# Kernel tuning notes

Hardware: AMD Instinct MI355X
Metric: run time of the kernel (lower is better)

## Reference

```python
import jax, jax.numpy as jnp
import numpy as np
from jax import lax

B, S, C_IN, D, H, P, W, DFF, K = 32, 4096, 32, 256, 8, 24, 64, 512, 5
DH = D // H
EPS = 1e-5


def _make_starts():
    stride = max(1, W // 2)
    idx = list(range(0, max(S - W + 1, 1), stride))
    if len(idx) == 0 or idx[-1] != S - W:
        if S - W >= 0:
            idx.append(S - W)
    return np.asarray(idx)

STARTS = _make_starts()                      # [M]
WIDX = STARTS[:, None] + np.arange(W)        # [M, W] patch gather indices


def setup_inputs() -> dict:
    key = jax.random.key(0)
    ks = jax.random.split(key, 24)
    r = lambda i, shape, s=0.02: (jax.random.normal(ks[i], shape, jnp.float32) * s)
    return {
        "x": jax.random.normal(ks[0], (B, S, C_IN), jnp.float32),
        "last_close_unused": jnp.zeros((B,), jnp.float32),
        "dw_w": r(1, (C_IN, 1, K), 0.2),      # depthwise conv kernel
        "pw_w": r(2, (D, C_IN), 0.1),         # pointwise conv (1x1)
        "bn_g": jnp.ones((D,), jnp.float32),
        "bn_b": jnp.zeros((D,), jnp.float32),
        "lg_Wq": r(3, (D, D)), "lg_Wk": r(4, (D, D)),
        "lg_Wv": r(5, (D, D)), "lg_Wo": r(6, (D, D)),
        "dec_Qd": r(7, (P, D), 1.0 / np.sqrt(D)),
        "dec_Wq": r(8, (D, D)), "dec_Wk": r(9, (D, D)),
        "dec_Wv": r(10, (D, D)), "dec_Wo": r(11, (D, D)),
        "ff1_w": r(12, (DFF, D)), "ff1_b": jnp.zeros((DFF,), jnp.float32),
        "ff2_w": r(13, (D, DFF)), "ff2_b": jnp.zeros((D,), jnp.float32),
        "out_w": r(14, (1, D)), "out_b": jnp.zeros((1,), jnp.float32),
        "gate_logits": jnp.tile(jnp.array([0.2, 0.4, 0.4], jnp.float32), (P, 1)),
    }


def _ln(x):
    m = x.mean(-1, keepdims=True)
    v = ((x - m) ** 2).mean(-1, keepdims=True)
    return (x - m) / jnp.sqrt(v + EPS)


def _split(t):  # [B, L, D] -> [B, H, L, DH]
    return t.reshape(t.shape[0], -1, H, DH).transpose(0, 2, 1, 3)


def _mha(Q, KV, Wq, Wk, Wv, scale):
    q = _split(Q @ Wq.T)
    k = _split(KV @ Wk.T)
    v = _split(KV @ Wv.T)
    attn = jax.nn.softmax(jnp.einsum('bhqd,bhkd->bhqk', q, k) * scale, axis=-1)
    o = jnp.einsum('bhqk,bhkd->bhqd', attn, v)
    o = o.transpose(0, 2, 1, 3).reshape(Q.shape[0], -1, D)
    return o, attn


def reference(x, last_close_unused, dw_w, pw_w, bn_g, bn_b,
              lg_Wq, lg_Wk, lg_Wv, lg_Wo,
              dec_Qd, dec_Wq, dec_Wk, dec_Wv, dec_Wo,
              ff1_w, ff1_b, ff2_w, ff2_b, out_w, out_b, gate_logits):
    # --- DepthwisePointwise front-end ---
    xt = jnp.transpose(x, (0, 2, 1))                         # [B, C, S]
    z = lax.conv_general_dilated(xt, dw_w, (1,), [(K // 2, K // 2)],
                                 dimension_numbers=('NCH', 'OIH', 'NCH'),
                                 feature_group_count=C_IN)
    z = jnp.einsum('dc,bcs->bds', pw_w, z)                   # pointwise 1x1
    z = jax.nn.gelu(z, approximate=False)
    m = z.mean((0, 2), keepdims=True)                        # BatchNorm1d (batch stats)
    v = ((z - m) ** 2).mean((0, 2), keepdims=True)
    z = (z - m) / jnp.sqrt(v + EPS) * bn_g[None, :, None] + bn_b[None, :, None]
    z = jnp.transpose(z, (0, 2, 1))                          # [B, S, D]

    # --- LocalGlobalAttention: patch-mean queries over full sequence K/V ---
    Q = z[:, WIDX].mean(axis=2)                              # [B, M, D]
    scale = 1.0 / np.sqrt(DH)
    o, attn_g = _mha(Q, z, lg_Wq, lg_Wk, lg_Wv, scale)
    Hh = _ln(o @ lg_Wo.T + Q)                                # [B, M, D]

    # --- CrossDecoder: learned queries ---
    Qd = jnp.broadcast_to(dec_Qd[None], (B, P, D))
    o2, attn_d = _mha(Qd, Hh, dec_Wq, dec_Wk, dec_Wv, scale)
    z2 = _ln(o2 @ dec_Wo.T + Qd)
    u = jax.nn.gelu(z2 @ ff1_w.T + ff1_b, approximate=False)
    u = _ln(u @ ff2_w.T + ff2_b + z2)
    y_global = (u @ out_w.T + out_b)[..., 0]                 # [B, P]

    # --- Gated combine: residual=0, local=global ---
    g = jax.nn.softmax(gate_logits, axis=-1)                 # [P, 3]
    y = g[:, 1][None, :] * y_global + g[:, 2][None, :] * y_global
    return (y, attn_g, attn_d)
```

## Files before the change

kernel.cpp:

```cpp
#include <hip/hip_runtime.h>
#include <hip/hip_bf16.h>
#include <cmath>

typedef unsigned short u16;
typedef __attribute__((ext_vector_type(4))) float f32x4;
typedef __attribute__((ext_vector_type(8))) short s16x8;

__device__ __forceinline__ float b2f(u16 u) { return __uint_as_float(((unsigned)u) << 16); }
__device__ __forceinline__ u16 f2b(float f) {
    unsigned u = __float_as_uint(f);
    unsigned r = (u + 0x7fffu + ((u >> 16) & 1u)) >> 16;
    return (u16)r;
}
__device__ __forceinline__ float gelu_f(float x) {
    float t = x * (0.7978845608f + 0.0356774081f * x * x);
    float e = exp2f(2.885390082f * t);
    return 0.5f * x * (1.0f + (e - 1.0f) / (e + 1.0f));
}

#define FOLD 0.25503590f

__global__ __launch_bounds__(256) void prep0_k(const float* __restrict__ pw_w,
        const float* __restrict__ lg_Wq, const float* __restrict__ lg_Wo,
        const float* __restrict__ dec_Wk, const float* __restrict__ dec_Wv,
// ... 58 lines not shown
    s16x8 bf[4];
    #pragma unroll
    for (int ni = 0; ni < 4; ++ni)
        bf[ni] = *(const s16x8*)(pwb + (n0 + ni * 16 + l16) * 32 + hi * 8);

    float cl[4] = {0,0,0,0}, ch[4] = {0,0,0,0};
    float ql[4] = {0,0,0,0}, qh[4] = {0,0,0,0};

    #pragma unroll
    for (int mi = 0; mi < 4; ++mi) {
        s16x8 af = *(const s16x8*)&As[mi * 16 + l16][hi * 8];
        #pragma unroll
        for (int ni = 0; ni < 4; ++ni) {
            f32x4 acc = __builtin_amdgcn_mfma_f32_16x16x32_bf16(af, bf[ni], zero, 0, 0, 0);
            int col = n0 + ni * 16 + l16;
            int rowb = r0 + mi * 16 + hi * 4;
            #pragma unroll
            for (int r = 0; r < 4; ++r) {
                float e = gelu_f(acc[r]);
                zp[(size_t)(rowb + r) * 256 + col] = f2b(e);
                if (mi < 2) { cl[ni] += e; ql[ni] += e * e; }
                else        { ch[ni] += e; qh[ni] += e * e; }
            }
        }
    }
    #pragma unroll
    for (int ni = 0; ni < 4; ++ni) {
        #pragma unroll
        for (int m = 16; m <= 32; m <<= 1) {
            cl[ni] += __shfl_xor(cl[ni], m);
            ch[ni] += __shfl_xor(ch[ni], m);
            ql[ni] += __shfl_xor(ql[ni], m);
            qh[ni] += __shfl_xor(qh[ni], m);
        }
        if (lane < 16) {
            int col = n0 + ni * 16 + lane;
            size_t bc = (size_t)(r0 >> 5);
            csum [bc * 256 + col]       = cl[ni];
            csum [(bc + 1) * 256 + col] = ch[ni];
            csum2[bc * 256 + col]       = ql[ni];
            csum2[(bc + 1) * 256 + col] = qh[ni];
        }
    }
}

__global__ __launch_bounds__(256) void stats2_k(const float* __restrict__ csum,
        const float* __restrict__ csum2, float* __restrict__ statp)
{
    int j = blockIdx.x, t = threadIdx.x;
    float s1 = 0, s2 = 0;
    for (int i = 0; i < 64; ++i) {
        s1 += csum [(size_t)(j * 64 + i) * 256 + t];
        s2 += csum2[(size_t)(j * 64 + i) * 256 + t];
    }
    statp[j * 512 + t] = s1;
    statp[j * 512 + 256 + t] = s2;
}

__global__ __launch_bounds__(256) void prep1_k(const float* __restrict__ statp,
        const float* __restrict__ bn_g, const float* __restrict__ bn_b,
        const float* __restrict__ gate_logits,
        float* __restrict__ a_ws, float* __restrict__ c_ws, float* __restrict__ coef)
{
    int t = threadIdx.x;
    float s1 = 0, s2 = 0;
    for (int j = 0; j < 64; ++j) {
        s1 += statp[j * 512 + t];
        s2 += statp[j * 512 + 256 + t];
    }
    const float invN = 1.0f / 131072.0f;
    float mean = s1 * invN;
    float var = s2 * invN - mean * mean;
    float av = bn_g[t] * rsqrtf(var + 1e-5f);
    a_ws[t] = av;
    c_ws[t] = bn_b[t] - mean * av;
    if (t < 24) {
        float g0 = gate_logits[t * 3], g1 = gate_logits[t * 3 + 1], g2 = gate_logits[t * 3 + 2];
        float mx = fmaxf(g0, fmaxf(g1, g2));
        float e0 = __expf(g0 - mx), e1 = __expf(g1 - mx), e2 = __expf(g2 - mx);
        coef[t] = (e1 + e2) / (e0 + e1 + e2);
    }
}

__global__ __launch_bounds__(256) void prep2b_k(const float* __restrict__ lg_Wk,
        const float* __restrict__ lg_Wv, const float* __restrict__ a_ws,
        const float* __restrict__ c_ws,
        u16* __restrict__ Wk_b, u16* __restrict__ Wv_b,
        float* __restrict__ betak, float* __restrict__ betav)
{
    __shared__ float red[4];
    int bid = blockIdx.x;
    int which = bid >> 8, row = bid & 255, t = threadIdx.x;
    const float* Wsrc = which ? lg_Wv : lg_Wk;
    float wv = Wsrc[row * 256 + t];
    (which ? Wv_b : Wk_b)[row * 256 + t] = f2b(wv * a_ws[t]);
    float v = wv * c_ws[t];
    for (int m = 32; m; m >>= 1) v += __shfl_xor(v, m);
    if ((t & 63) == 0) red[t >> 6] = v;
    __syncthreads();
    if (t == 0) (which ? betav : betak)[row] = red[0] + red[1] + red[2] + red[3];
}

__global__ __launch_bounds__(256) void q2_k(const float* __restrict__ dec_Qd,
        const float* __restrict__ dec_Wq, float* __restrict__ q2)
{
    __shared__ float wq[16][260];
    __shared__ float qd[24][260];
    int j = blockIdx.x, t = threadIdx.x;
    for (int idx = t; idx < 4096; idx += 256) {
        int tl = idx >> 8, d = idx & 255;
        wq[tl][d] = dec_Wq[(j * 16 + tl) * 256 + d];
    }
    for (int idx = t; idx < 6144; idx += 256) {
        int p = idx >> 8, d = idx & 255;
        qd[p][d] = dec_Qd[idx];
    }
    __syncthreads();
    for (int o = t; o < 384; o += 256) {
        int p = o >> 4, tl = o & 15;
        float s = 0;
        #pragma unroll 8
        for (int d = 0; d < 256; ++d) s += qd[p][d] * wq[tl][d];
        q2[p * 256 + j * 16 + tl] = s;
    }
}

__global__ __launch_bounds__(256) void qgemm_k(const float* __restrict__ csum,
        const float* __restrict__ a_ws, const float* __restrict__ c_ws,
        const u16* __restrict__ W, u16* __restrict__ qb)
{
    __shared__ u16 As[64 * 256];
    __shared__ float aa[256], ccx[256];
    const int t = threadIdx.x;
    const int r0 = blockIdx.x * 64;
    const int lane = t & 63, w = t >> 6;
    const int l16 = lane & 15, hi = lane >> 4;

    aa[t] = a_ws[t] * 0.015625f;
    ccx[t] = c_ws[t];
    __syncthreads();

    #pragma unroll
    for (int i = 0; i < 8; ++i) {
        int c = t + i * 256;
        int row = c >> 5, c16 = c & 31;
        int g = r0 + row, mm = g & 127;
        u16 tmp[8];
        if (mm == 127) {
            #pragma unroll
            for (int j = 0; j < 8; ++j) tmp[j] = 0;
        } else {
            const float* c0p = csum + (size_t)g * 256 + c16 * 8;
            const float* c1p = c0p + 256;
            #pragma unroll
            for (int j = 0; j < 8; ++j) {
                int d = c16 * 8 + j;
                tmp[j] = f2b((c0p[j] + c1p[j]) * aa[d] + ccx[d]);
            }
        }
        int boff = (c16 * 16) ^ ((row & 7) << 4);
        *(s16x8*)((char*)As + row * 512 + boff) = *(s16x8*)tmp;
    }
    __syncthreads();

    const int n0 = w * 64;
    f32x4 zero = {0, 0, 0, 0};
    f32x4 acc[4][4];
    #pragma unroll
    for (int mi = 0; mi < 4; ++mi)
        #pragma unroll
        for (int ni = 0; ni < 4; ++ni) acc[mi][ni] = zero;

    #pragma unroll
    for (int kk = 0; kk < 8; ++kk) {
        s16x8 af[4], bf[4];
        #pragma unroll
        for (int mi = 0; mi < 4; ++mi) {
            int row = mi * 16 + l16;
            int boff = (kk * 64 + hi * 16) ^ ((row & 7) << 4);
            af[mi] = *(const s16x8*)((const char*)As + row * 512 + boff);
        }
        #pragma unroll
        for (int ni = 0; ni < 4; ++ni)
            bf[ni] = *(const s16x8*)(W + (n0 + ni * 16 + l16) * 256 + kk * 32 + hi * 8);
        #pragma unroll
        for (int mi = 0; mi < 4; ++mi)
            #pragma unroll
            for (int ni = 0; ni < 4; ++ni)
                acc[mi][ni] = __builtin_amdgcn_mfma_f32_16x16x32_bf16(af[mi], bf[ni], acc[mi][ni], 0, 0, 0);
    }

    #pragma unroll
    for (int mi = 0; mi < 4; ++mi)
        #pragma unroll
        for (int ni = 0; ni < 4; ++ni) {
            int col = n0 + ni * 16 + l16;
            int rowb = r0 + mi * 16 + hi * 4;
            #pragma unroll
            for (int r = 0; r < 4; ++r)
                qb[(size_t)(rowb + r) * 256 + col] = f2b(acc[mi][ni][r] * FOLD);
        }
}

__global__ __launch_bounds__(256) void kv_k(const u16* __restrict__ zp,
        const u16* __restrict__ Wk, const u16* __restrict__ Wv,
        const float* __restrict__ betak, const float* __restrict__ betav,
        u16* __restrict__ kb, u16* __restrict__ vT)
{
    __shared__ __align__(16) char smem[36864];
    u16* As = (u16*)smem;
    const int t = threadIdx.x;
    const int r0 = blockIdx.x * 64;
    const int lane = t & 63, w = t >> 6;
    const int l16 = lane & 15, hi = lane >> 4;

    const u16* Ag = zp + (size_t)r0 * 256;
    #pragma unroll
    for (int i = 0; i < 8; ++i) {
        int c = t + i * 256;
        int row = c >> 5, c16 = c & 31;
        s16x8 v = *(const s16x8*)(Ag + row * 256 + c16 * 8);
        int boff = (c16 * 16) ^ ((row & 7) << 4);
        *(s16x8*)(smem + row * 512 + boff) = v;
    }
    __syncthreads();

    const int n0 = w * 64;
    f32x4 zero = {0, 0, 0, 0};
    f32x4 acc[4][4];
    #pragma unroll
    for (int mi = 0; mi < 4; ++mi)
        #pragma unroll
        for (int ni = 0; ni < 4; ++ni) acc[mi][ni] = zero;

    #pragma unroll
    for (int kk = 0; kk < 8; ++kk) {
        s16x8 af[4], bfk[4];
        #pragma unroll
        for (int mi = 0; mi < 4; ++mi) {
            int row = mi * 16 + l16;
            int boff = (kk * 64 + hi * 16) ^ ((row & 7) << 4);
            af[mi] = *(const s16x8*)(smem + row * 512 + boff);
        }
        #pragma unroll
        for (int ni = 0; ni < 4; ++ni)
            bfk[ni] = *(const s16x8*)(Wk + (n0 + ni * 16 + l16) * 256 + kk * 32 + hi * 8);
        #pragma unroll
        for (int mi = 0; mi < 4; ++mi)
            #pragma unroll
            for (int ni = 0; ni < 4; ++ni)
                acc[mi][ni] = __builtin_amdgcn_mfma_f32_16x16x32_bf16(af[mi], bfk[ni], acc[mi][ni], 0, 0, 0);
    }
    #pragma unroll
    for (int mi = 0; mi < 4; ++mi)
        #pragma unroll
        for (int ni = 0; ni < 4; ++ni) {
            int col = n0 + ni * 16 + l16;
            float bv = betak[col];
            int rowb = r0 + mi * 16 + hi * 4;
            #pragma unroll
            for (int r = 0; r < 4; ++r)
                kb[(size_t)(rowb + r) * 256 + col] = f2b(acc[mi][ni][r] + bv);
        }

    #pragma unroll
    for (int mi = 0; mi < 4; ++mi)
        #pragma unroll
        for (int ni = 0; ni < 4; ++ni) acc[mi][ni] = zero;
    #pragma unroll
    for (int kk = 0; kk < 8; ++kk) {
        s16x8 af[4], bfv[4];
        #pragma unroll
        for (int mi = 0; mi < 4; ++mi) {
            int row = mi * 16 + l16;
            int boff = (kk * 64 + hi * 16) ^ ((row & 7) << 4);
            af[mi] = *(const s16x8*)(smem + row * 512 + boff);
        }
        #pragma unroll
        for (int ni = 0; ni < 4; ++ni)
            bfv[ni] = *(const s16x8*)(Wv + (n0 + ni * 16 + l16) * 256 + kk * 32 + hi * 8);
        #pragma unroll
        for (int mi = 0; mi < 4; ++mi)
            #pragma unroll
            for (int ni = 0; ni < 4; ++ni)
                acc[mi][ni] = __builtin_amdgcn_mfma_f32_16x16x32_bf16(af[mi], bfv[ni], acc[mi][ni], 0, 0, 0);
    }
    __syncthreads();
    #pragma unroll
    for (int mi = 0; mi < 4; ++mi)
        #pragma unroll
        for (int ni = 0; ni < 4; ++ni) {
            int col = n0 + ni * 16 + l16;
            float bv = betav[col];
// ... 142 lines not shown
            for (int ni = 0; ni < 4; ++ni)
                acc[mi][ni] = __builtin_amdgcn_mfma_f32_16x16x32_bf16(af[mi], bf[ni], acc[mi][ni], 0, 0, 0);
    }
    #pragma unroll
    for (int mi = 0; mi < 4; ++mi)
        #pragma unroll
        for (int ni = 0; ni < 4; ++ni) {
            int col = n0 + ni * 16 + l16;
            int rowb = r0 + mi * 16 + hi * 4;
            #pragma unroll
            for (int r = 0; r < 4; ++r)
                C[(size_t)(rowb + r) * 256 + col] = f2b(acc[mi][ni][r]);
        }
}

__global__ __launch_bounds__(512) void attn_p1(const u16* __restrict__ qb,
        const u16* __restrict__ kb, const u16* __restrict__ vT,
        float* __restrict__ den, float* __restrict__ o_part)
{
    const int bid = blockIdx.x;
    const int b = bid >> 6, h = (bid >> 3) & 7, chunk = bid & 7;
    const int t = threadIdx.x, w = t >> 6, lane = t & 63;
    const int l16 = lane & 15, hi = lane >> 4;

    __shared__ u16 p_lds[8][16][48];

    s16x8 qf = *(const s16x8*)(qb + ((size_t)(b * 128 + w * 16 + l16)) * 256 + h * 32 + hi * 8);
    const u16* kbase = kb + (size_t)b * 4096 * 256 + h * 32 + hi * 8;
    const u16* vbase = vT + (size_t)(b * 8 + h) * 131072 + hi * 8;

    float dacc[4] = {0, 0, 0, 0};
    f32x4 zero = {0, 0, 0, 0};
    f32x4 oacc[2]; oacc[0] = zero; oacc[1] = zero;

    const int sbeg = chunk * 512, send = sbeg + 512;
    s16x8 kf0 = *(const s16x8*)(kbase + (size_t)(sbeg + l16) * 256);
    s16x8 kf1 = *(const s16x8*)(kbase + (size_t)(sbeg + 16 + l16) * 256);
    s16x8 vf0 = *(const s16x8*)(vbase + (sbeg >> 6) * 2048 + l16 * 64 + (sbeg & 63));
    s16x8 vf1 = *(const s16x8*)(vbase + (sbeg >> 6) * 2048 + (16 + l16) * 64 + (sbeg & 63));

    for (int s0 = sbeg; s0 < send; s0 += 32) {
        s16x8 k0 = kf0, k1 = kf1, v0 = vf0, v1 = vf1;
        int sn = s0 + 32;
        if (sn < send) {
            kf0 = *(const s16x8*)(kbase + (size_t)(sn + l16) * 256);
            kf1 = *(const s16x8*)(kbase + (size_t)(sn + 16 + l16) * 256);
            vf0 = *(const s16x8*)(vbase + (sn >> 6) * 2048 + l16 * 64 + (sn & 63));
            vf1 = *(const s16x8*)(vbase + (sn >> 6) * 2048 + (16 + l16) * 64 + (sn & 63));
        }
        f32x4 lg0 = __builtin_amdgcn_mfma_f32_16x16x32_bf16(qf, k0, zero, 0, 0, 0);
        f32x4 lg1 = __builtin_amdgcn_mfma_f32_16x16x32_bf16(qf, k1, zero, 0, 0, 0);
        #pragma unroll
        for (int r = 0; r < 4; ++r) {
            float e0 = exp2f(lg0[r]);
            float e1 = exp2f(lg1[r]);
            dacc[r] += e0 + e1;
            p_lds[w][hi * 4 + r][l16] = f2b(e0);
            p_lds[w][hi * 4 + r][16 + l16] = f2b(e1);
        }
        s16x8 pf = *(const s16x8*)(&p_lds[w][l16][hi * 8]);
        oacc[0] = __builtin_amdgcn_mfma_f32_16x16x32_bf16(pf, v0, oacc[0], 0, 0, 0);
        oacc[1] = __builtin_amdgcn_mfma_f32_16x16x32_bf16(pf, v1, oacc[1], 0, 0, 0);
    }

    #pragma unroll
    for (int m = 1; m <= 8; m <<= 1) {
        #pragma unroll
        for (int r = 0; r < 4; ++r) dacc[r] += __shfl_xor(dacc[r], m);
    }
    if (l16 == 0) {
        #pragma unroll
        for (int r = 0; r < 4; ++r)
            den[(size_t)chunk * 32768 + (b * 8 + h) * 128 + w * 16 + hi * 4 + r] = dacc[r];
    }
    #pragma unroll
    for (int vi = 0; vi < 2; ++vi)
        #pragma unroll
        for (int r = 0; r < 4; ++r) {
            int mg = w * 16 + hi * 4 + r;
            o_part[(size_t)chunk * 1048576 + (size_t)(b * 128 + mg) * 256 + h * 32 + vi * 16 + l16] = oacc[vi][r];
        }
}

__global__ __launch_bounds__(256) void dinv_k(const float* __restrict__ den, float* __restrict__ den_inv)
{
    int i = blockIdx.x * 256 + threadIdx.x;
    float s = 0;
    #pragma unroll
    for (int c = 0; c < 8; ++c) s += den[(size_t)c * 32768 + i];
    den_inv[i] = 1.0f / s;
}

__global__ __launch_bounds__(256) void norm_k(const float* __restrict__ o_part,
        const float* __restrict__ den_inv, u16* __restrict__ ob)
{
    int idx4 = blockIdx.x * 256 + threadIdx.x;
    int row = idx4 >> 6;
    int col4 = (idx4 & 63) * 4;
    int b = row >> 7, m = row & 127, h = col4 >> 5;
    float4 s = {0, 0, 0, 0};
    #pragma unroll
    for (int c = 0; c < 8; ++c) {
        float4 v = *(const float4*)(o_part + (size_t)c * 1048576 + (size_t)row * 256 + col4);
        s.x += v.x; s.y += v.y; s.z += v.z; s.w += v.w;
    }
    float rinv = den_inv[b * 1024 + h * 128 + m];
    ushort4 o;
    o.x = f2b(s.x * rinv); o.y = f2b(s.y * rinv);
    o.z = f2b(s.z * rinv); o.w = f2b(s.w * rinv);
    *(ushort4*)(ob + (size_t)row * 256 + col4) = o;
}

__global__ __launch_bounds__(512) void attn_p2(const u16* __restrict__ qb,
        const u16* __restrict__ kb, const float* __restrict__ den_inv,
        float* __restrict__ attn_out)
{
    const int bid = blockIdx.x;
    const int b = bid >> 6, h = (bid >> 3) & 7, chunk = bid & 7;
    const int t = threadIdx.x, w = t >> 6, lane = t & 63;
    const int l16 = lane & 15, hi = lane >> 4;

    __shared__ float buf[8][16][68];

    s16x8 qf = *(const s16x8*)(qb + ((size_t)(b * 128 + w * 16 + l16)) * 256 + h * 32 + hi * 8);
    const u16* kbase = kb + (size_t)b * 4096 * 256 + h * 32 + hi * 8;

    float rinv[4];
    #pragma unroll
    for (int r = 0; r < 4; ++r)
        rinv[r] = den_inv[b * 1024 + h * 128 + w * 16 + hi * 4 + r];

    f32x4 zero = {0, 0, 0, 0};
    float* ab = attn_out + (size_t)(b * 8 + h) * 127 * 4096;
    const int srow = lane >> 4;
    const int scol = (lane & 15) * 4;

    const int sbeg = chunk * 512, send = sbeg + 512;
    for (int s0 = sbeg; s0 < send; s0 += 64) {
        #pragma unroll
        for (int kk = 0; kk < 4; ++kk) {
            int sg = s0 + kk * 16 + l16;
            s16x8 kf = *(const s16x8*)(kbase + (size_t)sg * 256);
            f32x4 lg = __builtin_amdgcn_mfma_f32_16x16x32_bf16(qf, kf, zero, 0, 0, 0);
            #pragma unroll
            for (int r = 0; r < 4; ++r)
                buf[w][hi * 4 + r][kk * 16 + l16] = exp2f(lg[r]) * rinv[r];
        }
        #pragma unroll
        for (int rb = 0; rb < 4; ++rb) {
            int row = rb * 4 + srow;
            int mg = w * 16 + row;
            float4 v = *(const float4*)&buf[w][row][scol];
            if (mg < 127)
                *(float4*)(ab + (size_t)mg * 4096 + s0 + scol) = v;
        }
    }
}

__global__ __launch_bounds__(256) void ln_hh(const float* __restrict__ og,
        const float* __restrict__ csum, const float* __restrict__ a_ws,
        const float* __restrict__ c_ws, u16* __restrict__ Hb)
{
    __shared__ float red[8];
    int row = blockIdx.x, t = threadIdx.x;
    int mm = row & 127;
    float qv = 0.0f;
    if (mm != 127)
        qv = (csum[(size_t)row * 256 + t] + csum[(size_t)(row + 1) * 256 + t]) *
             (0.015625f * a_ws[t]) + c_ws[t];
    float v = og[(size_t)row * 256 + t] + qv;
    float s = v;
    for (int m = 32; m; m >>= 1) s += __shfl_xor(s, m);
    if ((t & 63) == 0) red[t >> 6] = s;
    __syncthreads();
    float mean = (red[0] + red[1] + red[2] + red[3]) * (1.0f / 256.0f);
    __syncthreads();
    float d = v - mean;
    float q = d * d;
    for (int m = 32; m; m >>= 1) q += __shfl_xor(q, m);
    if ((t & 63) == 0) red[t >> 6] = q;
    __syncthreads();
    float var = (red[0] + red[1] + red[2] + red[3]) * (1.0f / 256.0f);
    Hb[(size_t)row * 256 + t] = f2b(d * rsqrtf(var + 1e-5f));
}

__global__ __launch_bounds__(256) void dec_attn_k(const float* __restrict__ q2,
        const u16* __restrict__ k2b, const u16* __restrict__ v2b,
        float* __restrict__ attn_d, u16* __restrict__ o2b)
{
    __shared__ float qs2[24 * 32];
    __shared__ float ks[128][33];
    __shared__ float vs[128][33];
    __shared__ float lg2[24 * 128];
    __shared__ float sinv[24];
    int bid = blockIdx.x, b = bid >> 3, h = bid & 7;
    int t = threadIdx.x;
    const float scale = 0.17677669529663687f;
    for (int idx = t; idx < 4096; idx += 256) {
        int row = idx >> 5, c = idx & 31;
        ks[row][c] = b2f(k2b[((size_t)(b * 128 + row)) * 256 + h * 32 + c]);
        vs[row][c] = b2f(v2b[((size_t)(b * 128 + row)) * 256 + h * 32 + c]);
    }
    for (int idx = t; idx < 768; idx += 256) {
        int p = idx >> 5, i = idx & 31;
        qs2[idx] = q2[p * 256 + h * 32 + i];
    }
    __syncthreads();
    for (int idx = t; idx < 3048; idx += 256) {
        int p = idx / 127, m = idx - p * 127;
        float s = 0;
        #pragma unroll 8
        for (int i = 0; i < 32; ++i) s += qs2[p * 32 + i] * ks[m][i];
        lg2[p * 128 + m] = __expf(s * scale);
    }
    __syncthreads();
    if (t < 24) {
        float s = 0;
        for (int m = 0; m < 127; ++m) s += lg2[t * 128 + m];
        sinv[t] = 1.0f / s;
    }
    __syncthreads();
    float* ad = attn_d + (size_t)bid * 24 * 127;
    for (int idx = t; idx < 3048; idx += 256) {
        int p = idx / 127, m = idx - p * 127;
        float av = lg2[p * 128 + m] * sinv[p];
        lg2[p * 128 + m] = av;
        ad[idx] = av;
    }
    __syncthreads();
    for (int idx = t; idx < 768; idx += 256) {
        int p = idx >> 5, dh = idx & 31;
        float s = 0;
        for (int m = 0; m < 127; ++m)
            s += lg2[p * 128 + m] * vs[m][dh];
        o2b[((size_t)(b * 24 + p)) * 256 + h * 32 + dh] = f2b(s);
    }
}

__global__ __launch_bounds__(256) void ln3_k(const float* __restrict__ og2,
        const float* __restrict__ dec_Qd, float* __restrict__ z2f, u16* __restrict__ z2b)
{
    __shared__ float red[8];
    int row = blockIdx.x, p = row % 24, t = threadIdx.x;
    float v = og2[(size_t)row * 256 + t] + dec_Qd[p * 256 + t];
    float s = v;
    for (int m = 32; m; m >>= 1) s += __shfl_xor(s, m);
    if ((t & 63) == 0) red[t >> 6] = s;
    __syncthreads();
    float mean = (red[0] + red[1] + red[2] + red[3]) * (1.0f / 256.0f);
    __syncthreads();
    float d = v - mean, q = d * d;
    for (int m = 32; m; m >>= 1) q += __shfl_xor(q, m);
    if ((t & 63) == 0) red[t >> 6] = q;
    __syncthreads();
    float var = (red[0] + red[1] + red[2] + red[3]) * (1.0f / 256.0f);
    float u = d * rsqrtf(var + 1e-5f);
    z2f[(size_t)row * 256 + t] = u;
    z2b[(size_t)row * 256 + t] = f2b(u);
}

__global__ __launch_bounds__(256) void ln5_k(const float* __restrict__ uraw,
        const float* __restrict__ z2f, const float* __restrict__ out_w,
        const float* __restrict__ out_b, const float* __restrict__ coef,
        float* __restrict__ y)
{
    __shared__ float red[8];
    int row = blockIdx.x, p = row % 24, t = threadIdx.x;
    float v = uraw[(size_t)row * 256 + t] + z2f[(size_t)row * 256 + t];
    float s = v;
    for (int m = 32; m; m >>= 1) s += __shfl_xor(s, m);
    if ((t & 63) == 0) red[t >> 6] = s;
    __syncthreads();
    float mean = (red[0] + red[1] + red[2] + red[3]) * (1.0f / 256.0f);
    __syncthreads();
    float d = v - mean, q = d * d;
    for (int m = 32; m; m >>= 1) q += __shfl_xor(q, m);
    if ((t & 63) == 0) red[t >> 6] = q;
    __syncthreads();
    float var = (red[0] + red[1] + red[2] + red[3]) * (1.0f / 256.0f);
    float u = d * rsqrtf(var + 1e-5f);
    __syncthreads();
    float yp = u * out_w[t];
    for (int m = 32; m; m >>= 1) yp += __shfl_xor(yp, m);
    if ((t & 63) == 0) red[t >> 6] = yp;
    __syncthreads();
    if (t == 0) {
        float tot = red[0] + red[1] + red[2] + red[3] + out_b[0];
        y[row] = coef[p] * tot;
    }
}

extern "C" void kernel_launch(void* const* d_in, const int* in_sizes, int n_in,
                              void* d_out, int out_size, void* d_ws, size_t ws_size,
                              hipStream_t stream)
{
    const float* x        = (const float*)d_in[0];
    const float* dw_w     = (const float*)d_in[2];
    const float* pw_w     = (const float*)d_in[3];
    const float* bn_g     = (const float*)d_in[4];
    const float* bn_b     = (const float*)d_in[5];
    const float* lg_Wq    = (const float*)d_in[6];
    const float* lg_Wk    = (const float*)d_in[7];
    const float* lg_Wv    = (const float*)d_in[8];
    const float* lg_Wo    = (const float*)d_in[9];
    const float* dec_Qd   = (const float*)d_in[10];
    const float* dec_Wq   = (const float*)d_in[11];
    const float* dec_Wk   = (const float*)d_in[12];
    const float* dec_Wv   = (const float*)d_in[13];
    const float* dec_Wo   = (const float*)d_in[14];
    const float* ff1_w    = (const float*)d_in[15];
    const float* ff1_b    = (const float*)d_in[16];
    const float* ff2_w    = (const float*)d_in[17];
    const float* ff2_b    = (const float*)d_in[18];
    const float* out_w    = (const float*)d_in[19];
    const float* out_b    = (const float*)d_in[20];
    const float* gate_lg  = (const float*)d_in[21];

    char* ws = (char*)d_ws;
    size_t off = 0;
    auto alloc = [&](size_t bytes) -> void* {
        void* p = ws + off;
        off = (off + bytes + 255) & ~(size_t)255;
        return p;
    };
    u16*   zp    = (u16*)  alloc(67108864);
    u16*   kb    = (u16*)  alloc(67108864);
    u16*   vT    = (u16*)  alloc(67108864);
    float* csum  = (float*)alloc(4194304);
    float* csum2 = (float*)alloc(4194304);
    u16*   qb    = (u16*)  alloc(2097152);
    u16*   ob    = (u16*)  alloc(2097152);
    float* og    = (float*)alloc(4194304);
    u16*   Hb    = (u16*)  alloc(2097152);
    u16*   k2b   = (u16*)  alloc(2097152);
    u16*   v2b   = (u16*)  alloc(2097152);
    float* o_part= (float*)alloc(33554432);
    u16*   o2b   = (u16*)  alloc(393216);
    float* og2   = (float*)alloc(786432);
    float* z2f   = (float*)alloc(786432);
    u16*   z2b   = (u16*)  alloc(393216);
    u16*   u1b   = (u16*)  alloc(786432);
    float* uraw  = (float*)alloc(786432);
    float* q2    = (float*)alloc(24576);
    float* den   = (float*)alloc(1048576);
    float* den_i = (float*)alloc(131072);
    float* statp = (float*)alloc(131072);
    float* a_ws  = (float*)alloc(1024);
    float* c_ws  = (float*)alloc(1024);
    float* betak = (float*)alloc(1024);
    float* betav = (float*)alloc(1024);
    float* coef  = (float*)alloc(256);
    u16*   pwb   = (u16*)  alloc(16384);
    u16*   Wk_b  = (u16*)  alloc(131072);
    u16*   Wv_b  = (u16*)  alloc(131072);
    u16*   Wq_b  = (u16*)  alloc(131072);
    u16*   Wo_b  = (u16*)  alloc(131072);
    u16*   Wk2_b = (u16*)  alloc(131072);
    u16*   Wv2_b = (u16*)  alloc(131072);
    u16*   Wo2b  = (u16*)  alloc(131072);
    u16*   ff1b  = (u16*)  alloc(262144);
    u16*   ff2b  = (u16*)  alloc(262144);

    float* y_out  = (float*)d_out;
    float* attn_g = y_out + 768;
    float* attn_d = attn_g + (size_t)32 * 8 * 127 * 4096;

    prep0_k<<<2336, 256, 0, stream>>>(pw_w, lg_Wq, lg_Wo, dec_Wk, dec_Wv, dec_Wo, ff1_w, ff2_w,
                                      pwb, Wq_b, Wo_b, Wk2_b, Wv2_b, Wo2b, ff1b, ff2b);
    dwpw_k<<<2048, 256, 0, stream>>>(x, dw_w, pwb, zp, csum, csum2);
    stats2_k<<<64, 256, 0, stream>>>(csum, csum2, statp);
    prep1_k<<<1, 256, 0, stream>>>(statp, bn_g, bn_b, gate_lg, a_ws, c_ws, coef);
    prep2b_k<<<512, 256, 0, stream>>>(lg_Wk, lg_Wv, a_ws, c_ws, Wk_b, Wv_b, betak, betav);
    q2_k<<<16, 256, 0, stream>>>(dec_Qd, dec_Wq, q2);
    qgemm_k<<<64, 256, 0, stream>>>(csum, a_ws, c_ws, Wq_b, qb);
    kv_k<<<2048, 256, 0, stream>>>(zp, Wk_b, Wv_b, betak, betav, kb, vT);
    attn_p1<<<2048, 512, 0, stream>>>(qb, kb, vT, den, o_part);
    dinv_k<<<128, 256, 0, stream>>>(den, den_i);
    norm_k<<<1024, 256, 0, stream>>>(o_part, den_i, ob);
    attn_p2<<<2048, 512, 0, stream>>>(qb, kb, den_i, attn_g);
    gemm_g<1><<<64, 256, 0, stream>>>(ob, Wo_b, nullptr, og, 256, 1);
    ln_hh<<<4096, 256, 0, stream>>>(og, csum, a_ws, c_ws, Hb);
    gemm_dual<<<128, 256, 0, stream>>>(Hb, Wk2_b, Wv2_b, k2b, v2b);
    dec_attn_k<<<256, 256, 0, stream>>>(q2, k2b, v2b, attn_d, o2b);
    gemm_g<1><<<12, 256, 0, stream>>>(o2b, Wo2b, nullptr, og2, 256, 1);
    ln3_k<<<768, 256, 0, stream>>>(og2, dec_Qd, z2f, z2b);
    gemm_g<2><<<24, 256, 0, stream>>>(z2b, ff1b, ff1_b, u1b, 256, 2);
    gemm_g<1><<<12, 256, 0, stream>>>(u1b, ff2b, ff2_b, uraw, 512, 1);
    ln5_k<<<768, 256, 0, stream>>>(uraw, z2f, out_w, out_b, coef, y_out);
}
```

Before: 563.5 us.

## Fuse small prep kernels and merge layernorms into GEMM epilogues

Merges the prep2b, q2 and qgemm kernels into one launch that branches on block index, and folds the denominator reciprocal into norm_k and attn_p2 so dinv_k is gone. The three post-GEMM layernorm kernels (ln_hh, ln3, ln5) become epilogues of their GEMMs through a shared-memory staging tile, which drops the fp32 intermediate buffers. This removes several kernel launches and global round-trips on the small tail stages. In exchange the layernorm work now runs on far fewer blocks (64 or 12), and the denominator sum over chunks is recomputed in every thread.

After: 601.2 us. 6.7% more time.

```diff
diff --git a/kernel.cpp b/kernel.cpp
--- a/kernel.cpp
+++ b/kernel.cpp
@@ -164,124 +164,116 @@
     }
 }
 
-__global__ __launch_bounds__(256) void prep2b_k(const float* __restrict__ lg_Wk,
+__global__ __launch_bounds__(256) void prepx_k(const float* __restrict__ lg_Wk,
         const float* __restrict__ lg_Wv, const float* __restrict__ a_ws,
-        const float* __restrict__ c_ws,
+        const float* __restrict__ c_ws, const float* __restrict__ dec_Qd,
+        const float* __restrict__ dec_Wq, const float* __restrict__ csum,
+        const u16* __restrict__ Wq_b,
         u16* __restrict__ Wk_b, u16* __restrict__ Wv_b,
-        float* __restrict__ betak, float* __restrict__ betav)
-{
-    __shared__ float red[4];
-    int bid = blockIdx.x;
-    int which = bid >> 8, row = bid & 255, t = threadIdx.x;
-    const float* Wsrc = which ? lg_Wv : lg_Wk;
-    float wv = Wsrc[row * 256 + t];
-    (which ? Wv_b : Wk_b)[row * 256 + t] = f2b(wv * a_ws[t]);
-    float v = wv * c_ws[t];
-    for (int m = 32; m; m >>= 1) v += __shfl_xor(v, m);
-    if ((t & 63) == 0) red[t >> 6] = v;
-    __syncthreads();
-    if (t == 0) (which ? betav : betak)[row] = red[0] + red[1] + red[2] + red[3];
-}
-
-__global__ __launch_bounds__(256) void q2_k(const float* __restrict__ dec_Qd,
-        const float* __restrict__ dec_Wq, float* __restrict__ q2)
-{
-    __shared__ float wq[16][260];
-    __shared__ float qd[24][260];
-    int j = blockIdx.x, t = threadIdx.x;
-    for (int idx = t; idx < 4096; idx += 256) {
-        int tl = idx >> 8, d = idx & 255;
-        wq[tl][d] = dec_Wq[(j * 16 + tl) * 256 + d];
-    }
-    for (int idx = t; idx < 6144; idx += 256) {
-        int p = idx >> 8, d = idx & 255;
-        qd[p][d] = dec_Qd[idx];
-    }
-    __syncthreads();
-    for (int o = t; o < 384; o += 256) {
-        int p = o >> 4, tl = o & 15;
-        float s = 0;
-        #pragma unroll 8
-        for (int d = 0; d < 256; ++d) s += qd[p][d] * wq[tl][d];
-        q2[p * 256 + j * 16 + tl] = s;
-    }
-}
-
-__global__ __launch_bounds__(256) void qgemm_k(const float* __restrict__ csum,
-        const float* __restrict__ a_ws, const float* __restrict__ c_ws,
-        const u16* __restrict__ W, u16* __restrict__ qb)
-{
-    __shared__ u16 As[64 * 256];
-    __shared__ float aa[256], ccx[256];
-    const int t = threadIdx.x;
-    const int r0 = blockIdx.x * 64;
-    const int lane = t & 63, w = t >> 6;
-    const int l16 = lane & 15, hi = lane >> 4;
-
-    aa[t] = a_ws[t] * 0.015625f;
-    ccx[t] = c_ws[t];
-    __syncthreads();
-
-    #pragma unroll
-    for (int i = 0; i < 8; ++i) {
-        int c = t + i * 256;
-        int row = c >> 5, c16 = c & 31;
-        int g = r0 + row, mm = g & 127;
-        u16 tmp[8];
-        if (mm == 127) {
-            #pragma unroll
-            for (int j = 0; j < 8; ++j) tmp[j] = 0;
-        } else {
-            const float* c0p = csum + (size_t)g * 256 + c16 * 8;
-            const float* c1p = c0p + 256;
-            #pragma unroll
-            for (int j = 0; j < 8; ++j) {
-                int d = c16 * 8 + j;
-                tmp[j] = f2b((c0p[j] + c1p[j]) * aa[d] + ccx[d]);
+        float* __restrict__ betak, float* __restrict__ betav,
+        float* __restrict__ q2, u16* __restrict__ qb)
+{
+    __shared__ __align__(16) char sm[41728];
+    const int bid = blockIdx.x, t = threadIdx.x;
+    if (bid < 512) {
+        float* red = (float*)sm;
+        int which = bid >> 8, row = bid & 255;
+        const float* Wsrc = which ? lg_Wv : lg_Wk;
+        float wv = Wsrc[row * 256 + t];
+        (which ? Wv_b : Wk_b)[row * 256 + t] = f2b(wv * a_ws[t]);
+        float v = wv * c_ws[t];
+        for (int m = 32; m; m >>= 1) v += __shfl_xor(v, m);
+        if ((t & 63) == 0) red[t >> 6] = v;
+        __syncthreads();
+        if (t == 0) (which ? betav : betak)[row] = red[0] + red[1] + red[2] + red[3];
+    } else if (bid < 528) {
+        float (*wq)[260] = (float(*)[260])sm;
+        float (*qd)[260] = (float(*)[260])(sm + 16640);
+        int j = bid - 512;
+        for (int idx = t; idx < 4096; idx += 256) {
+            int tl = idx >> 8, d = idx & 255;
+            wq[tl][d] = dec_Wq[(j * 16 + tl) * 256 + d];
+        }
+        for (int idx = t; idx < 6144; idx += 256) {
+            int p = idx >> 8, d = idx & 255;
+            qd[p][d] = dec_Qd[idx];
+        }
+        __syncthreads();
+        for (int o = t; o < 384; o += 256) {
+            int p = o >> 4, tl = o & 15;
+            float s = 0;
+            #pragma unroll 8
+            for (int d = 0; d < 256; ++d) s += qd[p][d] * wq[tl][d];
+            q2[p * 256 + j * 16 + tl] = s;
+        }
+    } else {
+        u16* As = (u16*)sm;
+        float* aa = (float*)(sm + 32768);
+        float* ccx = (float*)(sm + 33792);
+        const int r0 = (bid - 528) * 64;
+        const int lane = t & 63, w = t >> 6;
+        const int l16 = lane & 15, hi = lane >> 4;
+        aa[t] = a_ws[t] * 0.015625f;
+        ccx[t] = c_ws[t];
+        __syncthreads();
+        #pragma unroll
+        for (int i = 0; i < 8; ++i) {
+            int c = t + i * 256;
+            int row = c >> 5, c16 = c & 31;
+            int g = r0 + row, mm = g & 127;
+            u16 tmp[8];
+            if (mm == 127) {
+                #pragma unroll
+                for (int j = 0; j < 8; ++j) tmp[j] = 0;
+            } else {
+                const float* c0p = csum + (size_t)g * 256 + c16 * 8;
+                const float* c1p = c0p + 256;
+                #pragma unroll
+                for (int j = 0; j < 8; ++j) {
+                    int d = c16 * 8 + j;
+                    tmp[j] = f2b((c0p[j] + c1p[j]) * aa[d] + ccx[d]);
+                }
             }
-        }
-        int boff = (c16 * 16) ^ ((row & 7) << 4);
-        *(s16x8*)((char*)As + row * 512 + boff) = *(s16x8*)tmp;
-    }
-    __syncthreads();
-
-    const int n0 = w * 64;
-    f32x4 zero = {0, 0, 0, 0};
-    f32x4 acc[4][4];
-    #pragma unroll
-    for (int mi = 0; mi < 4; ++mi)
-        #pragma unroll
-        for (int ni = 0; ni < 4; ++ni) acc[mi][ni] = zero;
-
-    #pragma unroll
-    for (int kk = 0; kk < 8; ++kk) {
-        s16x8 af[4], bf[4];
-        #pragma unroll
-        for (int mi = 0; mi < 4; ++mi) {
-            int row = mi * 16 + l16;
-            int boff = (kk * 64 + hi * 16) ^ ((row & 7) << 4);
-            af[mi] = *(const s16x8*)((const char*)As + row * 512 + boff);
-        }
-        #pragma unroll
-        for (int ni = 0; ni < 4; ++ni)
-            bf[ni] = *(const s16x8*)(W + (n0 + ni * 16 + l16) * 256 + kk * 32 + hi * 8);
+            int boff = (c16 * 16) ^ ((row & 7) << 4);
+            *(s16x8*)((char*)As + row * 512 + boff) = *(s16x8*)tmp;
+        }
+        __syncthreads();
+        const int n0 = w * 64;
+        f32x4 zero = {0, 0, 0, 0};
+        f32x4 acc[4][4];
         #pragma unroll
         for (int mi = 0; mi < 4; ++mi)
             #pragma unroll
+            for (int ni = 0; ni < 4; ++ni) acc[mi][ni] = zero;
+        #pragma unroll
+        for (int kk = 0; kk < 8; ++kk) {
+            s16x8 af[4], bf[4];
+            #pragma unroll
+            for (int mi = 0; mi < 4; ++mi) {
+                int row = mi * 16 + l16;
+                int boff = (kk * 64 + hi * 16) ^ ((row & 7) << 4);
+                af[mi] = *(const s16x8*)((const char*)As + row * 512 + boff);
+            }
+            #pragma unroll
             for (int ni = 0; ni < 4; ++ni)
-                acc[mi][ni] = __builtin_amdgcn_mfma_f32_16x16x32_bf16(af[mi], bf[ni], acc[mi][ni], 0, 0, 0);
-    }
-
-    #pragma unroll
-    for (int mi = 0; mi < 4; ++mi)
-        #pragma unroll
-        for (int ni = 0; ni < 4; ++ni) {
-            int col = n0 + ni * 16 + l16;
-            int rowb = r0 + mi * 16 + hi * 4;
-            #pragma unroll
-            for (int r = 0; r < 4; ++r)
-                qb[(size_t)(rowb + r) * 256 + col] = f2b(acc[mi][ni][r] * FOLD);
-        }
+                bf[ni] = *(const s16x8*)(Wq_b + (n0 + ni * 16 + l16) * 256 + kk * 32 + hi * 8);
+            #pragma unroll
+            for (int mi = 0; mi < 4; ++mi)
+                #pragma unroll
+                for (int ni = 0; ni < 4; ++ni)
+                    acc[mi][ni] = __builtin_amdgcn_mfma_f32_16x16x32_bf16(af[mi], bf[ni], acc[mi][ni], 0, 0, 0);
+        }
+        #pragma unroll
+        for (int mi = 0; mi < 4; ++mi)
+            #pragma unroll
+            for (int ni = 0; ni < 4; ++ni) {
+                int col = n0 + ni * 16 + l16;
+                int rowb = r0 + mi * 16 + hi * 4;
+                #pragma unroll
+                for (int r = 0; r < 4; ++r)
+                    qb[(size_t)(rowb + r) * 256 + col] = f2b(acc[mi][ni][r] * FOLD);
+            }
+    }
 }
 
 __global__ __launch_bounds__(256) void kv_k(const u16* __restrict__ zp,
@@ -290,7 +282,6 @@
         u16* __restrict__ kb, u16* __restrict__ vT)
 {
     __shared__ __align__(16) char smem[36864];
-    u16* As = (u16*)smem;
     const int t = threadIdx.x;
     const int r0 = blockIdx.x * 64;
     const int lane = t & 63, w = t >> 6;
@@ -599,37 +590,30 @@
         }
 }
 
-__global__ __launch_bounds__(256) void dinv_k(const float* __restrict__ den, float* __restrict__ den_inv)
-{
-    int i = blockIdx.x * 256 + threadIdx.x;
-    float s = 0;
-    #pragma unroll
-    for (int c = 0; c < 8; ++c) s += den[(size_t)c * 32768 + i];
-    den_inv[i] = 1.0f / s;
-}
-
 __global__ __launch_bounds__(256) void norm_k(const float* __restrict__ o_part,
-        const float* __restrict__ den_inv, u16* __restrict__ ob)
+        const float* __restrict__ den, u16* __restrict__ ob)
 {
     int idx4 = blockIdx.x * 256 + threadIdx.x;
     int row = idx4 >> 6;
     int col4 = (idx4 & 63) * 4;
     int b = row >> 7, m = row & 127, h = col4 >> 5;
-    float4 s = {0, 0, 0, 0};
-    #pragma unroll
-    for (int c = 0; c < 8; ++c) {
-        float4 v = *(const float4*)(o_part + (size_t)c * 1048576 + (size_t)row * 256 + col4);
-        s.x += v.x; s.y += v.y; s.z += v.z; s.w += v.w;
-    }
-    float rinv = den_inv[b * 1024 + h * 128 + m];
+    f32x4 s = {0, 0, 0, 0};
+    #pragma unroll
+    for (int c = 0; c < 8; ++c)
+        s += *(const f32x4*)(o_part + (size_t)c * 1048576 + (size_t)row * 256 + col4);
+    float ds = 0;
+    int di = (b * 8 + h) * 128 + m;
+    #pragma unroll
+    for (int c = 0; c < 8; ++c) ds += den[(size_t)c * 32768 + di];
+    float rinv = 1.0f / ds;
     ushort4 o;
-    o.x = f2b(s.x * rinv); o.y = f2b(s.y * rinv);
-    o.z = f2b(s.z * rinv); o.w = f2b(s.w * rinv);
+    o.x = f2b(s[0] * rinv); o.y = f2b(s[1] * rinv);
+    o.z = f2b(s[2] * rinv); o.w = f2b(s[3] * rinv);
     *(ushort4*)(ob + (size_t)row * 256 + col4) = o;
 }
 
 __global__ __launch_bounds__(512) void attn_p2(const u16* __restrict__ qb,
-        const u16* __restrict__ kb, const float* __restrict__ den_inv,
+        const u16* __restrict__ kb, const float* __restrict__ den,
         float* __restrict__ attn_out)
 {
     const int bid = blockIdx.x;
@@ -644,8 +628,13 @@
 
     float rinv[4];
     #pragma unroll
-    for (int r = 0; r < 4; ++r)
-        rinv[r] = den_inv[b * 1024 + h * 128 + w * 16 + hi * 4 + r];
+    for (int r = 0; r < 4; ++r) {
+        int di = (b * 8 + h) * 128 + w * 16 + hi * 4 + r;
+        float ds = 0;
+        #pragma unroll
+        for (int c = 0; c < 8; ++c) ds += den[(size_t)c * 32768 + di];
+        rinv[r] = 1.0f / ds;
+    }
 
     f32x4 zero = {0, 0, 0, 0};
     float* ab = attn_out + (size_t)(b * 8 + h) * 127 * 4096;
@@ -667,38 +656,102 @@
         for (int rb = 0; rb < 4; ++rb) {
             int row = rb * 4 + srow;
             int mg = w * 16 + row;
-            float4 v = *(const float4*)&buf[w][row][scol];
+            f32x4 v = *(const f32x4*)&buf[w][row][scol];
             if (mg < 127)
-                *(float4*)(ab + (size_t)mg * 4096 + s0 + scol) = v;
-        }
-    }
-}
-
-__global__ __launch_bounds__(256) void ln_hh(const float* __restrict__ og,
-        const float* __restrict__ csum, const float* __restrict__ a_ws,
-        const float* __restrict__ c_ws, u16* __restrict__ Hb)
-{
-    __shared__ float red[8];
-    int row = blockIdx.x, t = threadIdx.x;
-    int mm = row & 127;
-    float qv = 0.0f;
-    if (mm != 127)
-        qv = (csum[(size_t)row * 256 + t] + csum[(size_t)(row + 1) * 256 + t]) *
-             (0.015625f * a_ws[t]) + c_ws[t];
-    float v = og[(size_t)row * 256 + t] + qv;
-    float s = v;
-    for (int m = 32; m; m >>= 1) s += __shfl_xor(s, m);
-    if ((t & 63) == 0) red[t >> 6] = s;
-    __syncthreads();
-    float mean = (red[0] + red[1] + red[2] + red[3]) * (1.0f / 256.0f);
-    __syncthreads();
-    float d = v - mean;
-    float q = d * d;
-    for (int m = 32; m; m >>= 1) q += __shfl_xor(q, m);
-    if ((t & 63) == 0) red[t >> 6] = q;
-    __syncthreads();
-    float var = (red[0] + red[1] + red[2] + red[3]) * (1.0f / 256.0f);
-    Hb[(size_t)row * 256 + t] = f2b(d * rsqrtf(var + 1e-5f));
+                *(f32x4*)(ab + (size_t)mg * 4096 + s0 + scol) = v;
+        }
+    }
+}
+
+__global__ __launch_bounds__(256) void gemm_lnhh(const u16* __restrict__ A,
+        const u16* __restrict__ W, const float* __restrict__ csum,
+        const float* __restrict__ a_ws, const float* __restrict__ c_ws,
+        u16* __restrict__ Hb)
+{
+    __shared__ __align__(16) char sm[67584];
+    __shared__ float aa[256], cc2[256];
+    u16* As = (u16*)sm;
+    float (*Cs)[264] = (float(*)[264])sm;
+    const int t = threadIdx.x;
+    const int r0 = blockIdx.x * 64;
+    const int lane = t & 63, w = t >> 6;
+    const int l16 = lane & 15, hi = lane >> 4;
+
+    aa[t] = a_ws[t] * 0.015625f;
+    cc2[t] = c_ws[t];
+
+    const u16* Ag = A + (size_t)r0 * 256;
+    #pragma unroll
+    for (int i = 0; i < 8; ++i) {
+        int c = t + i * 256;
+        int row = c >> 5, c16 = c & 31;
+        s16x8 v = *(const s16x8*)(Ag + row * 256 + c16 * 8);
+        int boff = (c16 * 16) ^ ((row & 7) << 4);
+        *(s16x8*)(sm + row * 512 + boff) = v;
+    }
+    __syncthreads();
+
+    const int n0 = w * 64;
+    f32x4 zero = {0, 0, 0, 0};
+    f32x4 acc[4][4];
+    #pragma unroll
+    for (int mi = 0; mi < 4; ++mi)
+        #pragma unroll
+        for (int ni = 0; ni < 4; ++ni) acc[mi][ni] = zero;
+    #pragma unroll
+    for (int kk = 0; kk < 8; ++kk) {
+        s16x8 af[4], bf[4];
+        #pragma unroll
+        for (int mi = 0; mi < 4; ++mi) {
+            int row = mi * 16 + l16;
+            int boff = (kk * 64 + hi * 16) ^ ((row & 7) << 4);
+            af[mi] = *(const s16x8*)(sm + row * 512 + boff);
+        }
+        #pragma unroll
+        for (int ni = 0; ni < 4; ++ni)
+            bf[ni] = *(const s16x8*)(W + (n0 + ni * 16 + l16) * 256 + kk * 32 + hi * 8);
+        #pragma unroll
+        for (int mi = 0; mi < 4; ++mi)
+            #pragma unroll
+            for (int ni = 0; ni < 4; ++ni)
+                acc[mi][ni] = __builtin_amdgcn_mfma_f32_16x16x32_bf16(af[mi], bf[ni], acc[mi][ni], 0, 0, 0);
+    }
+    __syncthreads();
+    #pragma unroll
+    for (int mi = 0; mi < 4; ++mi)
+        #pragma unroll
+        for (int ni = 0; ni < 4; ++ni) {
+            int col = n0 + ni * 16 + l16;
+            int rowb = mi * 16 + hi * 4;
+            #pragma unroll
+            for (int r = 0; r < 4; ++r)
+                Cs[rowb + r][col] = acc[mi][ni][r];
+        }
+    __syncthreads();
+    for (int pass = 0; pass < 16; ++pass) {
+        int row = pass * 4 + w;
+        int g = r0 + row, mm = g & 127;
+        float v[4];
+        #pragma unroll
+        for (int j = 0; j < 4; ++j) {
+            int d = lane + j * 64;
+            float qv = 0.0f;
+            if (mm != 127)
+                qv = (csum[(size_t)g * 256 + d] + csum[(size_t)(g + 1) * 256 + d]) * aa[d] + cc2[d];
+            v[j] = Cs[row][d] + qv;
+        }
+        float s = v[0] + v[1] + v[2] + v[3];
+        for (int m = 32; m; m >>= 1) s += __shfl_xor(s, m);
+        float mean = s * (1.0f / 256.0f);
+        float q = 0;
+        #pragma unroll
+        for (int j = 0; j < 4; ++j) { float d_ = v[j] - mean; q += d_ * d_; }
+        for (int m = 32; m; m >>= 1) q += __shfl_xor(q, m);
+        float rs = rsqrtf(q * (1.0f / 256.0f) + 1e-5f);
+        #pragma unroll
+        for (int j = 0; j < 4; ++j)
+            Hb[(size_t)g * 256 + lane + j * 64] = f2b((v[j] - mean) * rs);
+    }
 }
 
 __global__ __launch_bounds__(256) void dec_attn_k(const float* __restrict__ q2,
@@ -754,56 +807,182 @@
     }
 }
 
-__global__ __launch_bounds__(256) void ln3_k(const float* __restrict__ og2,
-        const float* __restrict__ dec_Qd, float* __restrict__ z2f, u16* __restrict__ z2b)
-{
-    __shared__ float red[8];
-    int row = blockIdx.x, p = row % 24, t = threadIdx.x;
-    float v = og2[(size_t)row * 256 + t] + dec_Qd[p * 256 + t];
-    float s = v;
-    for (int m = 32; m; m >>= 1) s += __shfl_xor(s, m);
-    if ((t & 63) == 0) red[t >> 6] = s;
-    __syncthreads();
-    float mean = (red[0] + red[1] + red[2] + red[3]) * (1.0f / 256.0f);
-    __syncthreads();
-    float d = v - mean, q = d * d;
-    for (int m = 32; m; m >>= 1) q += __shfl_xor(q, m);
-    if ((t & 63) == 0) red[t >> 6] = q;
-    __syncthreads();
-    float var = (red[0] + red[1] + red[2] + red[3]) * (1.0f / 256.0f);
-    float u = d * rsqrtf(var + 1e-5f);
-    z2f[(size_t)row * 256 + t] = u;
-    z2b[(size_t)row * 256 + t] = f2b(u);
-}
-
-__global__ __launch_bounds__(256) void ln5_k(const float* __restrict__ uraw,
+__global__ __launch_bounds__(256) void gemm_ln3(const u16* __restrict__ A,
+        const u16* __restrict__ W, const float* __restrict__ dec_Qd,
+        float* __restrict__ z2f, u16* __restrict__ z2b)
+{
+    __shared__ __align__(16) char sm[67584];
+    u16* As = (u16*)sm;
+    float (*Cs)[264] = (float(*)[264])sm;
+    const int t = threadIdx.x;
+    const int r0 = blockIdx.x * 64;
+    const int lane = t & 63, w = t >> 6;
+    const int l16 = lane & 15, hi = lane >> 4;
+
+    const u16* Ag = A + (size_t)r0 * 256;
+    #pragma unroll
+    for (int i = 0; i < 8; ++i) {
+        int c = t + i * 256;
+        int row = c >> 5, c16 = c & 31;
+        s16x8 v = *(const s16x8*)(Ag + row * 256 + c16 * 8);
+        int boff = (c16 * 16) ^ ((row & 7) << 4);
+        *(s16x8*)(sm + row * 512 + boff) = v;
+    }
+    __syncthreads();
+
+    const int n0 = w * 64;
+    f32x4 zero = {0, 0, 0, 0};
+    f32x4 acc[4][4];
+    #pragma unroll
+    for (int mi = 0; mi < 4; ++mi)
+        #pragma unroll
+        for (int ni = 0; ni < 4; ++ni) acc[mi][ni] = zero;
+    #pragma unroll
+    for (int kk = 0; kk < 8; ++kk) {
+        s16x8 af[4], bf[4];
+        #pragma unroll
+        for (int mi = 0; mi < 4; ++mi) {
+            int row = mi * 16 + l16;
+            int boff = (kk * 64 + hi * 16) ^ ((row & 7) << 4);
+            af[mi] = *(const s16x8*)(sm + row * 512 + boff);
+        }
+        #pragma unroll
+        for (int ni = 0; ni < 4; ++ni)
+            bf[ni] = *(const s16x8*)(W + (n0 + ni * 16 + l16) * 256 + kk * 32 + hi * 8);
+        #pragma unroll
+        for (int mi = 0; mi < 4; ++mi)
+            #pragma unroll
+            for (int ni = 0; ni < 4; ++ni)
+                acc[mi][ni] = __builtin_amdgcn_mfma_f32_16x16x32_bf16(af[mi], bf[ni], acc[mi][ni], 0, 0, 0);
+    }
+    __syncthreads();
+    #pragma unroll
+    for (int mi = 0; mi < 4; ++mi)
+        #pragma unroll
+        for (int ni = 0; ni < 4; ++ni) {
+            int col = n0 + ni * 16 + l16;
+            int rowb = mi * 16 + hi * 4;
+            #pragma unroll
+            for (int r = 0; r < 4; ++r)
+                Cs[rowb + r][col] = acc[mi][ni][r];
+        }
+    __syncthreads();
+    for (int pass = 0; pass < 16; ++pass) {
+        int row = pass * 4 + w;
+        int g = r0 + row, p = g % 24;
+        float v[4];
+        #pragma unroll
+        for (int j = 0; j < 4; ++j) {
+            int d = lane + j * 64;
+            v[j] = Cs[row][d] + dec_Qd[p * 256 + d];
+        }
+        float s = v[0] + v[1] + v[2] + v[3];
+        for (int m = 32; m; m >>= 1) s += __shfl_xor(s, m);
+        float mean = s * (1.0f / 256.0f);
+        float q = 0;
+        #pragma unroll
+        for (int j = 0; j < 4; ++j) { float d_ = v[j] - mean; q += d_ * d_; }
+        for (int m = 32; m; m >>= 1) q += __shfl_xor(q, m);
+        float rs = rsqrtf(q * (1.0f / 256.0f) + 1e-5f);
+        #pragma unroll
+        for (int j = 0; j < 4; ++j) {
+            float u = (v[j] - mean) * rs;
+            z2f[(size_t)g * 256 + lane + j * 64] = u;
+            z2b[(size_t)g * 256 + lane + j * 64] = f2b(u);
+        }
+    }
+}
+
+__global__ __launch_bounds__(256) void gemm_ln5(const u16* __restrict__ A,
+        const u16* __restrict__ W, const float* __restrict__ bias,
         const float* __restrict__ z2f, const float* __restrict__ out_w,
         const float* __restrict__ out_b, const float* __restrict__ coef,
         float* __restrict__ y)
 {
-    __shared__ float red[8];
-    int row = blockIdx.x, p = row % 24, t = threadIdx.x;
-    float v = uraw[(size_t)row * 256 + t] + z2f[(size_t)row * 256 + t];
-    float s = v;
-    for (int m = 32; m; m >>= 1) s += __shfl_xor(s, m);
-    if ((t & 63) == 0) red[t >> 6] = s;
-    __syncthreads();
-    float mean = (red[0] + red[1] + red[2] + red[3]) * (1.0f / 256.0f);
-    __syncthreads();
-    float d = v - mean, q = d * d;
-    for (int m = 32; m; m >>= 1) q += __shfl_xor(q, m);
-    if ((t & 63) == 0) red[t >> 6] = q;
-    __syncthreads();
-    float var = (red[0] + red[1] + red[2] + red[3]) * (1.0f / 256.0f);
-    float u = d * rsqrtf(var + 1e-5f);
-    __syncthreads();
-    float yp = u * out_w[t];
-    for (int m = 32; m; m >>= 1) yp += __shfl_xor(yp, m);
-    if ((t & 63) == 0) red[t >> 6] = yp;
-    __syncthreads();
-    if (t == 0) {
-        float tot = red[0] + red[1] + red[2] + red[3] + out_b[0];
-        y[row] = coef[p] * tot;
+    __shared__ __align__(16) char sm[67584];
+    u16* As = (u16*)sm;
+    float (*Cs)[264] = (float(*)[264])sm;
+    const int t = threadIdx.x;
+    const int r0 = blockIdx.x * 64;
+    const int lane = t & 63, w = t >> 6;
+    const int l16 = lane & 15, hi = lane >> 4;
+    const int K = 512;
+
+    const u16* Ag = A + (size_t)r0 * K;
+    const int n0 = w * 64;
+    f32x4 zero = {0, 0, 0, 0};
+    f32x4 acc[4][4];
+    #pragma unroll
+    for (int mi = 0; mi < 4; ++mi)
+        #pragma unroll
+        for (int ni = 0; ni < 4; ++ni) acc[mi][ni] = zero;
+
+    for (int kc = 0; kc < K; kc += 256) {
+        if (kc) __syncthreads();
+        #pragma unroll
+        for (int i = 0; i < 8; ++i) {
+            int c = t + i * 256;
+            int row = c >> 5, c16 = c & 31;
+            s16x8 v = *(const s16x8*)(Ag + (size_t)row * K + kc + c16 * 8);
+            int boff = (c16 * 16) ^ ((row & 7) << 4);
+            *(s16x8*)(sm + row * 512 + boff) = v;
+        }
+        __syncthreads();
+        #pragma unroll
+        for (int kk = 0; kk < 8; ++kk) {
+            s16x8 af[4], bf[4];
+            #pragma unroll
+            for (int mi = 0; mi < 4; ++mi) {
+                int row = mi * 16 + l16;
+                int boff = (kk * 64 + hi * 16) ^ ((row & 7) << 4);
+                af[mi] = *(const s16x8*)(sm + row * 512 + boff);
+            }
+            #pragma unroll
+            for (int ni = 0; ni < 4; ++ni)
+                bf[ni] = *(const s16x8*)(W + (size_t)(n0 + ni * 16 + l16) * K + kc + kk * 32 + hi * 8);
+            #pragma unroll
+            for (int mi = 0; mi < 4; ++mi)
+                #pragma unroll
+                for (int ni = 0; ni < 4; ++ni)
+                    acc[mi][ni] = __builtin_amdgcn_mfma_f32_16x16x32_bf16(af[mi], bf[ni], acc[mi][ni], 0, 0, 0);
+        }
+    }
+    __syncthreads();
+    #pragma unroll
+    for (int mi = 0; mi < 4; ++mi)
+        #pragma unroll
+        for (int ni = 0; ni < 4; ++ni) {
+            int col = n0 + ni * 16 + l16;
+            int rowb = mi * 16 + hi * 4;
+            #pragma unroll
+            for (int r = 0; r < 4; ++r)
+                Cs[rowb + r][col] = acc[mi][ni][r];
+        }
+    __syncthreads();
+    for (int pass = 0; pass < 16; ++pass) {
+        int row = pass * 4 + w;
+        int g = r0 + row, p = g % 24;
+        float v[4];
+        #pragma unroll
+        for (int j = 0; j < 4; ++j) {
+            int d = lane + j * 64;
+            v[j] = Cs[row][d] + bias[d] + z2f[(size_t)g * 256 + d];
+        }
+        float s = v[0] + v[1] + v[2] + v[3];
+        for (int m = 32; m; m >>= 1) s += __shfl_xor(s, m);
+        float mean = s * (1.0f / 256.0f);
+        float q = 0;
+        #pragma unroll
+        for (int j = 0; j < 4; ++j) { float d_ = v[j] - mean; q += d_ * d_; }
+        for (int m = 32; m; m >>= 1) q += __shfl_xor(q, m);
+        float rs = rsqrtf(q * (1.0f / 256.0f) + 1e-5f);
+        float yp = 0;
+        #pragma unroll
+        for (int j = 0; j < 4; ++j)
+            yp += (v[j] - mean) * rs * out_w[lane + j * 64];
+        for (int m = 32; m; m >>= 1) yp += __shfl_xor(yp, m);
+        if (lane == 0)
+            y[g] = coef[p] * (yp + out_b[0]);
     }
 }
 
@@ -847,20 +1026,16 @@
     float* csum2 = (float*)alloc(4194304);
     u16*   qb    = (u16*)  alloc(2097152);
     u16*   ob    = (u16*)  alloc(2097152);
-    float* og    = (float*)alloc(4194304);
     u16*   Hb    = (u16*)  alloc(2097152);
     u16*   k2b   = (u16*)  alloc(2097152);
     u16*   v2b   = (u16*)  alloc(2097152);
     float* o_part= (float*)alloc(33554432);
     u16*   o2b   = (u16*)  alloc(393216);
-    float* og2   = (float*)alloc(786432);
     float* z2f   = (float*)alloc(786432);
     u16*   z2b   = (u16*)  alloc(393216);
     u16*   u1b   = (u16*)  alloc(786432);
-    float* uraw  = (float*)alloc(786432);
     float* q2    = (float*)alloc(24576);
     float* den   = (float*)alloc(1048576);
-    float* den_i = (float*)alloc(131072);
     float* statp = (float*)alloc(131072);
     float* a_ws  = (float*)alloc(1024);
     float* c_ws  = (float*)alloc(1024);
@@ -887,21 +1062,16 @@
     dwpw_k<<<2048, 256, 0, stream>>>(x, dw_w, pwb, zp, csum, csum2);
     stats2_k<<<64, 256, 0, stream>>>(csum, csum2, statp);
     prep1_k<<<1, 256, 0, stream>>>(statp, bn_g, bn_b, gate_lg, a_ws, c_ws, coef);
-    prep2b_k<<<512, 256, 0, stream>>>(lg_Wk, lg_Wv, a_ws, c_ws, Wk_b, Wv_b, betak, betav);
-    q2_k<<<16, 256, 0, stream>>>(dec_Qd, dec_Wq, q2);
-    qgemm_k<<<64, 256, 0, stream>>>(csum, a_ws, c_ws, Wq_b, qb);
+    prepx_k<<<592, 256, 0, stream>>>(lg_Wk, lg_Wv, a_ws, c_ws, dec_Qd, dec_Wq, csum, Wq_b,
+                                     Wk_b, Wv_b, betak, betav, q2, qb);
     kv_k<<<2048, 256, 0, stream>>>(zp, Wk_b, Wv_b, betak, betav, kb, vT);
     attn_p1<<<2048, 512, 0, stream>>>(qb, kb, vT, den, o_part);
-    dinv_k<<<128, 256, 0, stream>>>(den, den_i);
-    norm_k<<<1024, 256, 0, stream>>>(o_part, den_i, ob);
-    attn_p2<<<2048, 512, 0, stream>>>(qb, kb, den_i, attn_g);
-    gemm_g<1><<<64, 256, 0, stream>>>(ob, Wo_b, nullptr, og, 256, 1);
-    ln_hh<<<4096, 256, 0, stream>>>(og, csum, a_ws, c_ws, Hb);
+    norm_k<<<1024, 256, 0, stream>>>(o_part, den, ob);
+    attn_p2<<<2048, 512, 0, stream>>>(qb, kb, den, attn_g);
+    gemm_lnhh<<<64, 256, 0, stream>>>(ob, Wo_b, csum, a_ws, c_ws, Hb);
     gemm_dual<<<128, 256, 0, stream>>>(Hb, Wk2_b, Wv2_b, k2b, v2b);
     dec_attn_k<<<256, 256, 0, stream>>>(q2, k2b, v2b, attn_d, o2b);
-    gemm_g<1><<<12, 256, 0, stream>>>(o2b, Wo2b, nullptr, og2, 256, 1);
-    ln3_k<<<768, 256, 0, stream>>>(og2, dec_Qd, z2f, z2b);
+    gemm_ln3<<<12, 256, 0, stream>>>(o2b, Wo2b, dec_Qd, z2f, z2b);
     gemm_g<2><<<24, 256, 0, stream>>>(z2b, ff1b, ff1_b, u1b, 256, 2);
-    gemm_g<1><<<12, 256, 0, stream>>>(u1b, ff2b, ff2_b, uraw, 512, 1);
-    ln5_k<<<768, 256, 0, stream>>>(uraw, z2f, out_w, out_b, coef, y_out);
-}
+    gemm_ln5<<<12, 256, 0, stream>>>(u1b, ff2b, ff2_b, z2f, out_w, out_b, coef, y_out);
+}
```
